# Kernel optimization log

Hardware: AMD Instinct MI355X
Metric: run time of the kernel (lower is better)

The kernel has to match this reference:

```python
import jax, jax.numpy as jnp
import numpy as np

H = 8          # n_heads
C_FACTOR = 3   # autocorrelation factor c
KS = 25        # series-decomp moving-average kernel


def series_decomp(x, ks=KS):
    # AvgPool1d(kernel=ks, stride=1, pad=ks//2), count_include_pad=True (torch default)
    p = ks // 2
    xp = jnp.pad(x, ((0, 0), (p, p), (0, 0)))            # [B, L+2p, D]
    cs = jnp.pad(jnp.cumsum(xp, axis=1), ((0, 0), (1, 0), (0, 0)))
    trend = (cs[:, ks:, :] - cs[:, :-ks, :]) / ks         # [B, L, D]
    return x - trend, trend


def auto_correlation(x, Wq, bq, Wk, bk, Wv, bv):
    B, L, D = x.shape
    d = D // H

    def proj(W, b):  # [B,L,D] -> [B,H,L,d]
        return (x @ W + b).reshape(B, L, H, d).transpose(0, 2, 1, 3)

    Q, K, V = proj(Wq, bq), proj(Wk, bk), proj(Wv, bv)
    Qf = jnp.fft.rfft(Q, axis=2)
    Kf = jnp.fft.rfft(K, axis=2)
    Corr = jnp.fft.irfft(Qf * jnp.conj(Kf), n=L, axis=2)  # [B,H,L,d]

    k = int(C_FACTOR * np.log(L))                         # topk = int(c*log(L))
    C2 = Corr.transpose(0, 1, 3, 2)                       # [B,H,d,L] - topk along lag axis per channel
    W_topk, I_topk = jax.lax.top_k(C2, k)                 # [B,H,d,k]
    W_topk = jax.nn.softmax(W_topk, axis=-1)

    # saturating shift: pos = min(delay + t, L-1)  (faithful to clamp(max=L-1))
    t = jnp.arange(L)
    pos = jnp.minimum(I_topk[..., None] + t[None, None, None, None, :], L - 1)  # [B,H,d,k,L]
    Vt = V.transpose(0, 1, 3, 2)                          # [B,H,d,L]
    gathered = jnp.take_along_axis(Vt[:, :, :, None, :], pos, axis=4)           # [B,H,d,k,L]
    R = jnp.einsum('bhdk,bhdkl->bhdl', W_topk, gathered)  # weighted aggregate over lags
    return R.transpose(0, 3, 1, 2).reshape(B, L, D)       # [B,L,D]


def setup_inputs() -> dict:
    key = jax.random.key(0)
    ks = jax.random.split(key, 11)
    B, L, D = 8, 1024, 512
    s = 0.02
    return {
        'x':  jax.random.normal(ks[0], (B, L, D), jnp.float32),
        'Wq': jax.random.normal(ks[1], (D, D), jnp.float32) * s,
        'bq': jnp.zeros((D,), jnp.float32),
        'Wk': jax.random.normal(ks[2], (D, D), jnp.float32) * s,
        'bk': jnp.zeros((D,), jnp.float32),
        'Wv': jax.random.normal(ks[3], (D, D), jnp.float32) * s,
        'bv': jnp.zeros((D,), jnp.float32),
        'W1': jax.random.normal(ks[4], (D, D), jnp.float32) * s,
        'b1': jnp.zeros((D,), jnp.float32),
        'W2': jax.random.normal(ks[5], (D, D), jnp.float32) * s,
        'b2': jnp.zeros((D,), jnp.float32),
    }


def reference(x, Wq, bq, Wk, bk, Wv, bv, W1, b1, W2, b2):
    attn = auto_correlation(x, Wq, bq, Wk, bk, Wv, bv)
    x_s, _ = series_decomp(attn + x)
    y = jax.nn.relu(x_s @ W1 + b1) @ W2 + b2              # FFN (dropout is identity in eval)
    x_s, _ = series_decomp(y + x_s)
    return x_s
```

## Files before the change

kernel.cpp:

```cpp
#include <hip/hip_runtime.h>
#include <math.h>

#define LL 1024
#define DD 512
#define NB 8
#define KTOP 20
#define SZ (8 * 512 * 1024)

typedef __attribute__((ext_vector_type(8))) short bf16x8;
typedef __attribute__((ext_vector_type(4))) float f32x4;
typedef __attribute__((ext_vector_type(4))) int i32x4;

__device__ __forceinline__ unsigned short f2bf(float f) {
  union { float f; unsigned u; } v; v.f = f;
  unsigned r = v.u + 0x7FFFu + ((v.u >> 16) & 1u);
  return (unsigned short)(r >> 16);
}
__device__ __forceinline__ float bf2f(unsigned short u) {
  union { unsigned u; float f; } v; v.u = ((unsigned)u) << 16;
  return v.f;
}

__device__ __forceinline__ void gload16(const void* g, void* l) {
  __builtin_amdgcn_global_load_lds(
      (const __attribute__((address_space(1))) unsigned int*)g,
      (__attribute__((address_space(3))) unsigned int*)l, 16, 0, 0);
}

__global__ __launch_bounds__(256) void k_prep(const float* __restrict__ x,
                                              float* __restrict__ xT,
                                              unsigned short* __restrict__ xb,
                                              const float* __restrict__ Wq,
                                              const float* __restrict__ Wk,
                                              const float* __restrict__ Wv,
                                              const float* __restrict__ W1,
                                              const float* __restrict__ W2,
                                              const float* __restrict__ bq,
                                              const float* __restrict__ bk,
                                              const float* __restrict__ bv,
                                              unsigned short* __restrict__ WqkvT,
                                              unsigned short* __restrict__ W1T,
                                              unsigned short* __restrict__ W2T,
                                              float* __restrict__ bqkv) {
  __shared__ float T[64][65];
  int bid = blockIdx.x;
  int tid = threadIdx.x;
  int lane = tid & 63, r4 = tid >> 6;
  if (bid < 1024) {
    int b = bid >> 7, c0 = ((bid >> 4) & 7) * 64, t0 = (bid & 15) * 64;
#pragma unroll
    for (int it = 0; it < 16; ++it) {
      int tl = it * 4 + r4;
      T[lane][tl] = x[((size_t)b * LL + t0 + tl) * DD + c0 + lane];
    }
    __syncthreads();
#pragma unroll
    for (int it = 0; it < 16; ++it) {
      int cl = it * 4 + r4;
      xT[((size_t)b * DD + c0 + cl) * LL + t0 + lane] = T[cl][lane];
    }
    int tl2 = tid >> 2, cq = (tid & 3) * 16;
    unsigned short* dxb = xb + ((size_t)b * LL + t0 + tl2) * DD + c0 + cq;
#pragma unroll
    for (int j = 0; j < 16; j += 4) {
      ushort4 u;
      u.x = f2bf(T[cq + j][tl2]);
      u.y = f2bf(T[cq + j + 1][tl2]);
      u.z = f2bf(T[cq + j + 2][tl2]);
      u.w = f2bf(T[cq + j + 3][tl2]);
      *(ushort4*)&dxb[j] = u;
    }
  } else {
    int pid = bid - 1024;
    int z = pid >> 6, n0 = ((pid >> 3) & 7) * 64, k0 = (pid & 7) * 64;
    const float* W = (z == 0) ? Wq : (z == 1) ? Wk : (z == 2) ? Wv : (z == 3) ? W1 : W2;
    unsigned short* dst = (z == 0) ? WqkvT
                        : (z == 1) ? (WqkvT + 512 * 512)
                        : (z == 2) ? (WqkvT + 1024 * 512)
                        : (z == 3) ? W1T : W2T;
#pragma unroll
    for (int it = 0; it < 16; ++it) {
      int kl = it * 4 + r4;
      T[lane][kl] = W[(size_t)(k0 + kl) * DD + n0 + lane];
    }
    __syncthreads();
    int n = tid >> 2, kq = (tid & 3) * 16;
    unsigned short* d = dst + (size_t)(n0 + n) * DD + k0 + kq;
#pragma unroll
    for (int j = 0; j < 16; j += 4) {
      ushort4 u;
      u.x = f2bf(T[n][kq + j]);
      u.y = f2bf(T[n][kq + j + 1]);
      u.z = f2bf(T[n][kq + j + 2]);
      u.w = f2bf(T[n][kq + j + 3]);
      *(ushort4*)&d[j] = u;
    }
    if (z == 4 && n0 == 0 && k0 == 0) {
      for (int i = tid; i < 1536; i += 256) {
        const float* s = (i < 512) ? bq : (i < 1024) ? bk : bv;
        bqkv[i] = s[i & 511];
      }
    }
  }
}

template <int MODE>
__global__ __launch_bounds__(256) void k_mfma(const unsigned short* __restrict__ Aptr,
                                              const unsigned short* __restrict__ Bt,
                                              const float* __restrict__ bias,
                                              const unsigned short* __restrict__ resbT,
                                              unsigned short* __restrict__ outU,
                                              float* __restrict__ outF, int gx) {
  __shared__ char smem[34816];
  unsigned short* As = (unsigned short*)smem;
  unsigned short* Bs = (unsigned short*)(smem + 16384);
  float* Cs = (float*)smem;

  int tid = threadIdx.x;
  int lane = tid & 63, wid = tid >> 6;
  int wr = wid & 1, wc = wid >> 1;

  int nwg = gridDim.x;
  int wg = blockIdx.x;
  int swz = (wg & 7) * (nwg >> 3) + (wg >> 3);
  int bix = swz % gx, biy = swz / gx;
  int n0 = bix * 128, m0 = biy * 128;
  int b = m0 >> 10, t0 = m0 & (LL - 1);

  f32x4 acc[4][4];
#pragma unroll
  for (int i = 0; i < 4; ++i)
#pragma unroll
    for (int j = 0; j < 4; ++j) acc[i][j] = (f32x4){0.f, 0.f, 0.f, 0.f};

  int srow = tid >> 3, sq = tid & 7;

  for (int k0 = 0; k0 < 512; k0 += 64) {
#pragma unroll
    for (int p = 0; p < 4; ++p) {
      int r = srow + p * 32;
      int dq = sq ^ (r & 7);
      gload16(Aptr + (size_t)(m0 + r) * 512 + k0 + dq * 8, &As[r * 64 + sq * 8]);
      gload16(Bt + (size_t)(n0 + r) * 512 + k0 + dq * 8, &Bs[r * 64 + sq * 8]);
    }
    __syncthreads();
#pragma unroll
    for (int ks = 0; ks < 2; ++ks) {
      bf16x8 af[4], bf[4];
      int fr = lane & 15, kq = lane >> 4;
#pragma unroll
      for (int mi = 0; mi < 4; ++mi) {
        int r = wr * 64 + mi * 16 + fr;
        af[mi] = *(bf16x8*)&As[r * 64 + ((ks * 4 + kq) ^ (r & 7)) * 8];
      }
#pragma unroll
      for (int ni = 0; ni < 4; ++ni) {
        int r = wc * 64 + ni * 16 + fr;
        bf[ni] = *(bf16x8*)&Bs[r * 64 + ((ks * 4 + kq) ^ (r & 7)) * 8];
      }
#pragma unroll
      for (int mi = 0; mi < 4; ++mi)
#pragma unroll
        for (int ni = 0; ni < 4; ++ni)
          acc[mi][ni] = __builtin_amdgcn_mfma_f32_16x16x32_bf16(af[mi], bf[ni], acc[mi][ni], 0, 0, 0);
    }
    __syncthreads();
  }

  if (MODE == 0 || MODE == 2) {
    const int LDc = 132;
    for (int p = 0; p < 2; ++p) {
      __syncthreads();
      if (MODE == 2) {
        int n = tid >> 2, mq = tid & 3;
        const unsigned short* rrow =
            resbT + ((size_t)(b * 512) + n0 + p * 64 + n) * LL + t0;
#pragma unroll
        for (int i = 0; i < 8; ++i) {
          int m = mq * 4 + i * 16;
          ushort4 u = *(const ushort4*)&rrow[m];
          float4 v;
          v.x = bf2f(u.x); v.y = bf2f(u.y); v.z = bf2f(u.z); v.w = bf2f(u.w);
          *(float4*)&Cs[n * LDc + m] = v;
        }
        __syncthreads();
      }
      if (wc == p) {
#pragma unroll
        for (int mi = 0; mi < 4; ++mi)
#pragma unroll
          for (int ni = 0; ni < 4; ++ni) {
            int nl = ni * 16 + (lane & 15);
            int ml = wr * 64 + mi * 16 + (lane >> 4) * 4;
            if (MODE == 2) {
              f32x4 cur = *(f32x4*)&Cs[nl * LDc + ml];
              cur += acc[mi][ni];
              *(f32x4*)&Cs[nl * LDc + ml] = cur;
            } else {
              *(f32x4*)&Cs[nl * LDc + ml] = acc[mi][ni];
            }
          }
      }
      __syncthreads();
      {
        int n = tid >> 2, mq = tid & 3;
        int ng = n0 + p * 64 + n;
        float bv = bias[ng];
        if (MODE == 0) {
          int sel = ng >> 9;
          unsigned short* drow =
              outU + ((size_t)sel * NB * 512 + b * 512 + (ng & 511)) * LL + t0;
#pragma unroll
          for (int i = 0; i < 8; ++i) {
            int m = mq * 4 + i * 16;
            float4 v = *(float4*)&Cs[n * LDc + m];
            ushort4 u;
            u.x = f2bf(v.x + bv); u.y = f2bf(v.y + bv);
            u.z = f2bf(v.z + bv); u.w = f2bf(v.w + bv);
            *(ushort4*)&drow[m] = u;
          }
        } else {
          float* drow = outF + ((size_t)b * 512 + ng) * LL + t0;
#pragma unroll
          for (int i = 0; i < 8; ++i) {
            int m = mq * 4 + i * 16;
            float4 v = *(float4*)&Cs[n * LDc + m];
            v.x += bv; v.y += bv; v.z += bv; v.w += bv;
            *(float4*)&drow[m] = v;
          }
        }
      }
    }
  } else {
    const int LDh = 68;
    for (int p = 0; p < 2; ++p) {
      __syncthreads();
      if (wc == p) {
#pragma unroll
        for (int mi = 0; mi < 4; ++mi)
#pragma unroll
          for (int ni = 0; ni < 4; ++ni) {
            int nl = ni * 16 + (lane & 15);
            int ml = wr * 64 + mi * 16 + (lane >> 4) * 4;
#pragma unroll
            for (int r = 0; r < 4; ++r) Cs[(ml + r) * LDh + nl] = acc[mi][ni][r];
          }
      }
      __syncthreads();
      {
        int m = tid >> 1, nh = tid & 1;
        unsigned short* drow =
            outU + (size_t)(m0 + m) * 512 + n0 + p * 64 + nh * 32;
#pragma unroll
        for (int c = 0; c < 8; ++c) {
          float4 v = *(float4*)&Cs[m * LDh + nh * 32 + c * 4];
          float4 bb = *(const float4*)&bias[n0 + p * 64 + nh * 32 + c * 4];
          v.x = fmaxf(v.x + bb.x, 0.f);
          v.y = fmaxf(v.y + bb.y, 0.f);
          v.z = fmaxf(v.z + bb.z, 0.f);
          v.w = fmaxf(v.w + bb.w, 0.f);
          ushort4 u;
          u.x = f2bf(v.x); u.y = f2bf(v.y); u.z = f2bf(v.z); u.w = f2bf(v.w);
          *(ushort4*)&drow[c * 4] = u;
        }
      }
    }
  }
}

__global__ __launch_bounds__(256) void k_autocorr(const unsigned short* __restrict__ Qbf,
                                                  const unsigned short* __restrict__ Kbf,
                                                  const unsigned short* __restrict__ Vbf,
                                                  const float* __restrict__ xT,
                                                  unsigned short* __restrict__ xsbT) {
  __shared__ char sm[20768];
  unsigned* QsW  = (unsigned*)sm;
  unsigned* KshW = (unsigned*)(sm + 4096);
  float* Vs2 = (float*)(sm + 12416);
  float* Cp  = (float*)(sm + 4608);
  float* wvs = (float*)(sm + 20608);
  int*   wis = (int*)(sm + 20688);
  float* Csp = (float*)sm;

  int tid = threadIdx.x;
  int lane = tid & 63, wave = tid >> 6;
  size_t base = (size_t)blockIdx.x * LL;

  {
    ushort4 q = *(const ushort4*)(Qbf + base + tid * 4);
    unsigned q0 = (unsigned)q.x | ((unsigned)q.y << 16);
    unsigned q1 = (unsigned)q.z | ((unsigned)q.w << 16);
    int Wa = 2 * tid;
    int Pa = Wa ^ (((Wa >> 5) & 3) << 2);
    uint2 qv; qv.x = q0; qv.y = q1;
    *(uint2*)&QsW[Pa] = qv;
    int Wb = 512 + 2 * tid;
    int Pb = Wb ^ (((Wb >> 5) & 3) << 2);
    *(uint2*)&QsW[Pb] = qv;

    ushort4 vv = *(const ushort4*)(Vbf + base + tid * 4);
    float4 vf;
    vf.x = bf2f(vv.x); vf.y = bf2f(vv.y); vf.z = bf2f(vv.z); vf.w = bf2f(vv.w);
    *(float4*)&Vs2[tid * 4] = vf;
    float vlast = bf2f(Vbf[base + 1023]);
    *(float4*)&Vs2[1024 + tid * 4] = make_float4(vlast, vlast, vlast, vlast);

    ushort4 kv = *(const ushort4*)(Kbf + base + tid * 4);
    unsigned w0 = (unsigned)kv.x | ((unsigned)kv.y << 16);
    unsigned w1 = (unsigned)kv.z | ((unsigned)kv.w << 16);
    unsigned wq = __shfl_up(w0, 1);
    unsigned wp = __shfl_up(w1, 1);
    if (lane == 0) {
      wq = *(const unsigned*)(Kbf + base + ((tid * 4 - 4) & (LL - 1)));
      wp = *(const unsigned*)(Kbf + base + ((tid * 4 - 2) & (LL - 1)));
    }
    int d = 8 + 2 * tid;
    uint2 u0; u0.x = w0;                      u0.y = w1;
    uint2 u1; u1.x = (wp >> 16) | (w0 << 16); u1.y = (w0 >> 16) | (w1 << 16);
    uint2 u2; u2.x = wp;                      u2.y = w0;
    uint2 u3; u3.x = (wq >> 16) | (wp << 16); u3.y = (wp >> 16) | (w0 << 16);
    *(uint2*)&KshW[d]        = u0;
    *(uint2*)&KshW[520 + d]  = u1;
    *(uint2*)&KshW[1040 + d] = u2;
    *(uint2*)&KshW[1560 + d] = u3;
    if (tid >= 224) {
      int q2 = tid - 224;
      int s = q2 >> 3, dd = q2 & 7;
      int p = 2 * dd - 16;
      unsigned short a = Kbf[base + ((p - s) & (LL - 1))];
      unsigned short b2 = Kbf[base + ((p + 1 - s) & (LL - 1))];
      KshW[s * 520 + dd] = (unsigned)a | ((unsigned)b2 << 16);
    }
  }
  __syncthreads();

  f32x4 acc = (f32x4){0.f, 0.f, 0.f, 0.f};
  int fr = lane & 15, kq = lane >> 4;
  int g = wave;
  int srow = fr & 3, fp = fr >> 2;
  int aW0 = 128 * g + 8 * fr + 4 * kq;
  int bD0 = srow * 520 + 8 + 4 * kq - 2 * fp;
#pragma unroll
  for (int ks = 0; ks < 32; ++ks) {
    int W = aW0 + 16 * ks;
    int Pw = W ^ (((W >> 5) & 3) << 2);
    bf16x8 av = *(const bf16x8*)&QsW[Pw];
    int bD = bD0 + 16 * ks;
    uint2 b01 = *(const uint2*)&KshW[bD];
    uint2 b23 = *(const uint2*)&KshW[bD + 2];
    union { unsigned u[4]; bf16x8 h; } ub;
    ub.u[0] = b01.x; ub.u[1] = b01.y; ub.u[2] = b23.x; ub.u[3] = b23.y;
    acc = __builtin_amdgcn_mfma_f32_16x16x32_bf16(av, ub.h, acc, 0, 0, 0);
  }
  __syncthreads();
#pragma unroll
  for (int r = 0; r < 4; ++r) {
    int tau = 256 * g + 64 * kq + 16 * r + fr;
    Cp[tau ^ (((tau >> 6) & 3) << 4)] = acc[r];
  }
  __syncthreads();

  int sel = blockIdx.x & 3;
  if (wave == sel) {
    float c0[16];
#pragma unroll
    for (int j = 0; j < 16; ++j) {
      int tau = 64 * j + lane;
      c0[j] = Cp[tau ^ (((tau >> 6) & 3) << 4)];
    }
    float lbest = c0[0];
    int lidx = 0;
#pragma unroll
    for (int m = 1; m < 16; ++m)
      if (c0[m] > lbest) { lbest = c0[m]; lidx = m; }

    float wv[KTOP];
    int wiR[KTOP];
#pragma unroll
    for (int s = 0; s < KTOP; ++s) {
      float best = lbest;
      int bidx = 64 * lidx + lane;
#pragma unroll
      for (int off = 32; off; off >>= 1) {
        float v2 = __shfl_xor(best, off);
        int i2 = __shfl_xor(bidx, off);
        if (v2 > best || (v2 == best && i2 < bidx)) { best = v2; bidx = i2; }
      }
      wv[s] = best;
      wiR[s] = bidx;
      int kill = ((bidx & 63) == lane) ? (bidx >> 6) : -1;
#pragma unroll
      for (int m = 0; m < 16; ++m)
        if (m == kill) c0[m] = -3.0e38f;
      lbest = c0[0];
      lidx = 0;
#pragma unroll
      for (int m = 1; m < 16; ++m)
        if (c0[m] > lbest) { lbest = c0[m]; lidx = m; }
    }
    float mx = wv[0];
#pragma unroll
    for (int m = 1; m < KTOP; ++m) mx = fmaxf(mx, wv[m]);
    float ssum = 0.f;
#pragma unroll
    for (int m = 0; m < KTOP; ++m) {
      wv[m] = __expf(wv[m] - mx);
      ssum += wv[m];
    }
    float inv = 1.f / ssum;
    if (lane == 0) {
#pragma unroll
      for (int m = 0; m < KTOP; ++m) {
        wvs[m] = wv[m] * inv;
        wis[m] = wiR[m];
      }
    }
  } else {
    int ft = (wave < sel ? wave : wave - 1) * 64 + lane;
    if (ft < 16) Csp[ft] = 0.f;
    else if (ft < 32) Csp[1040 + ft - 16] = 0.f;
  }
  __syncthreads();

  {
    float r[4];
#pragma unroll
    for (int i = 0; i < 4; ++i) r[i] = xT[base + tid + 256 * i];
#pragma unroll
    for (int k = 0; k < KTOP; ++k) {
      float w = wvs[k];
      int wi = wis[k];
#pragma unroll
      for (int i = 0; i < 4; ++i) r[i] += w * Vs2[wi + tid + 256 * i];
    }
#pragma unroll
    for (int i = 0; i < 4; ++i) Csp[16 + tid + 256 * i] = r[i];
  }
  __syncthreads();

  {
    int t0 = tid * 4;
    float buf[28];
#pragma unroll
    for (int qd = 0; qd < 7; ++qd)
      *(float4*)&buf[qd * 4] = *(const float4*)&Csp[t0 + 4 + qd * 4];
    float s = 0.f;
#pragma unroll
    for (int m = 0; m < 25; ++m) s += buf[m];
    ushort4 o;
    o.x = f2bf(buf[12] - s * (1.0f / 25.0f));
    s += buf[25] - buf[0];
    o.y = f2bf(buf[13] - s * (1.0f / 25.0f));
    s += buf[26] - buf[1];
    o.z = f2bf(buf[14] - s * (1.0f / 25.0f));
    s += buf[27] - buf[2];
    o.w = f2bf(buf[15] - s * (1.0f / 25.0f));
    *(ushort4*)&xsbT[base + t0] = o;
  }
}

__global__ __launch_bounds__(256) void k_castT(const unsigned short* __restrict__ src,
                                               unsigned short* __restrict__ dst) {
  __shared__ unsigned short T[64][68];
  int b = blockIdx.z;
  int t0 = blockIdx.x * 64, c0 = blockIdx.y * 64;
  int tid = threadIdx.x;
  int lane = tid & 63, r4 = tid >> 6;
#pragma unroll
  for (int it = 0; it < 16; ++it) {
    int cl = it * 4 + r4;
    T[lane][cl] = src[((size_t)b * 512 + c0 + cl) * LL + t0 + lane];
  }
  __syncthreads();
  int tl = tid >> 2, cq = (tid & 3) * 16;
  unsigned short* d = dst + ((size_t)b * LL + t0 + tl) * 512 + c0 + cq;
#pragma unroll
  for (int j = 0; j < 16; j += 4) {
    ushort4 u;
    u.x = T[tl][cq + j]; u.y = T[tl][cq + j + 1];
    u.z = T[tl][cq + j + 2]; u.w = T[tl][cq + j + 3];
    *(ushort4*)&d[j] = u;
  }
}

#define DCH 32
__global__ __launch_bounds__(256) void k_decomp2T(const float* __restrict__ s2T,
                                                  float* __restrict__ out) {
  __shared__ float T[DCH][289];
  int b = blockIdx.z, c0 = blockIdx.y * DCH, t0 = blockIdx.x * 256;
  int tid = threadIdx.x;
  {
    int row = tid >> 3, j0 = tid & 7;
    const float* src = s2T + ((size_t)b * 512 + c0 + row) * LL;
#pragma unroll
    for (int i = 0; i < 9; ++i) {
      int col = (j0 + i * 8) * 4;
      int t = t0 - 16 + col;
      float4 v = make_float4(0.f, 0.f, 0.f, 0.f);
      if (t >= 0 && t < LL) v = *(const float4*)&src[t];
      *(float4*)&T[row][col] = v;
    }
  }
  __syncthreads();
  int c = tid & 31, tg = tid >> 5;
  float sum = 0.f;
  int basec = tg * 32 + 4;
#pragma unroll
  for (int j = 0; j < 25; ++j) sum += T[c][basec + j];
  float* orow = out + ((size_t)b * LL + t0 + tg * 32) * 512 + c0 + c;
#pragma unroll 1
  for (int s = 0; s < 32; ++s) {
    float center = T[c][tg * 32 + 16 + s];
    orow[(size_t)s * 512] = center - sum * (1.f / 25.f);
    sum += T[c][basec + 25 + s] - T[c][basec + s];
  }
}

extern "C" void kernel_launch(void* const* d_in, const int* in_sizes, int n_in,
                              void* d_out, int out_size, void* d_ws, size_t ws_size,
                              hipStream_t stream) {
  const float* x  = (const float*)d_in[0];
  const float* Wq = (const float*)d_in[1];
  const float* bq = (const float*)d_in[2];
  const float* Wk = (const float*)d_in[3];
  const float* bk = (const float*)d_in[4];
  const float* Wv = (const float*)d_in[5];
  const float* bv = (const float*)d_in[6];
  const float* W1 = (const float*)d_in[7];
  const float* b1 = (const float*)d_in[8];
  const float* W2 = (const float*)d_in[9];
  const float* b2 = (const float*)d_in[10];
  float* out = (float*)d_out;
  char* w = (char*)d_ws;

  float* xT             = (float*)w;
  unsigned short* Qbf   = (unsigned short*)(w + (size_t)SZ * 4);
  unsigned short* Kbf   = Qbf + SZ;
  unsigned short* Vbf   = Kbf + SZ;
  unsigned short* WqkvT = (unsigned short*)(w + (size_t)SZ * 12);
  unsigned short* W1T   = WqkvT + 1536 * 512;
  unsigned short* W2T   = W1T + 512 * 512;
  float* bqkv           = (float*)(W2T + 512 * 512);
  unsigned short* xb    = (unsigned short*)(w + (size_t)SZ * 14);
  unsigned short* h1    = (unsigned short*)w;
  unsigned short* xsb   = (unsigned short*)(w + (size_t)SZ * 2);
  unsigned short* xsbT  = Qbf;
  float* s2T            = (float*)(w + (size_t)SZ * 6);

  k_prep<<<dim3(1344), 256, 0, stream>>>(x, xT, xb, Wq, Wk, Wv, W1, W2,
                                         bq, bk, bv, WqkvT, W1T, W2T, bqkv);

  k_mfma<0><<<dim3(768), 256, 0, stream>>>(xb, WqkvT, bqkv, nullptr, Qbf, nullptr, 12);

  k_autocorr<<<dim3(NB * DD), 256, 0, stream>>>(Qbf, Kbf, Vbf, xT, xsbT);

  k_castT<<<dim3(16, 8, NB), 256, 0, stream>>>(xsbT, xsb);

  k_mfma<1><<<dim3(256), 256, 0, stream>>>(xsb, W1T, b1, nullptr, h1, nullptr, 4);
  k_mfma<2><<<dim3(256), 256, 0, stream>>>(h1, W2T, b2, xsbT, nullptr, s2T, 4);

  k_decomp2T<<<dim3(4, 16, NB), 256, 0, stream>>>(s2T, out);
}
```

Measured before the change: 152.4 us.

## Shrink autocorr LDS/registers: read Q from global, bf16 residual, lane-parallel softmax

The autocorrelation kernel stops staging Q in shared memory and reads MFMA A-fragments straight from global (L1/L2), which cuts LDS to about 16.7KB. Top-k results go to LDS per step instead of register arrays, and the softmax is computed across lanes with shuffles. The kernel now asks for 8 blocks per CU to raise occupancy. The transposed residual x is stored as bf16 instead of fp32, which halves its write and read traffic but adds rounding error to the residual path.

After: 139.7 us. -8.3%, faster.

```diff
diff --git a/kernel.cpp b/kernel.cpp
--- a/kernel.cpp
+++ b/kernel.cpp
@@ -28,7 +28,7 @@
 }
 
 __global__ __launch_bounds__(256) void k_prep(const float* __restrict__ x,
-                                              float* __restrict__ xT,
+                                              unsigned short* __restrict__ xbT,
                                               unsigned short* __restrict__ xb,
                                               const float* __restrict__ Wq,
                                               const float* __restrict__ Wk,
@@ -57,7 +57,7 @@
 #pragma unroll
     for (int it = 0; it < 16; ++it) {
       int cl = it * 4 + r4;
-      xT[((size_t)b * DD + c0 + cl) * LL + t0 + lane] = T[cl][lane];
+      xbT[((size_t)b * DD + c0 + cl) * LL + t0 + lane] = f2bf(T[cl][lane]);
     }
     int tl2 = tid >> 2, cq = (tid & 3) * 16;
     unsigned short* dxb = xb + ((size_t)b * LL + t0 + tl2) * DD + c0 + cq;
@@ -268,36 +268,24 @@
   }
 }
 
-__global__ __launch_bounds__(256) void k_autocorr(const unsigned short* __restrict__ Qbf,
-                                                  const unsigned short* __restrict__ Kbf,
-                                                  const unsigned short* __restrict__ Vbf,
-                                                  const float* __restrict__ xT,
-                                                  unsigned short* __restrict__ xsbT) {
-  __shared__ char sm[20768];
-  unsigned* QsW  = (unsigned*)sm;
-  unsigned* KshW = (unsigned*)(sm + 4096);
-  float* Vs2 = (float*)(sm + 12416);
-  float* Cp  = (float*)(sm + 4608);
-  float* wvs = (float*)(sm + 20608);
-  int*   wis = (int*)(sm + 20688);
+__global__ __launch_bounds__(256, 8) void k_autocorr(const unsigned short* __restrict__ Qbf,
+                                                     const unsigned short* __restrict__ Kbf,
+                                                     const unsigned short* __restrict__ Vbf,
+                                                     const unsigned short* __restrict__ xbT,
+                                                     unsigned short* __restrict__ xsbT) {
+  __shared__ char sm[16672];
+  unsigned* KshW = (unsigned*)sm;
+  float* Vs2 = (float*)(sm + 8320);
+  float* wvs = (float*)(sm + 16512);
+  int*   wis = (int*)(sm + 16592);
   float* Csp = (float*)sm;
+  float* Cp  = (float*)(sm + 4224);
 
   int tid = threadIdx.x;
   int lane = tid & 63, wave = tid >> 6;
   size_t base = (size_t)blockIdx.x * LL;
 
   {
-    ushort4 q = *(const ushort4*)(Qbf + base + tid * 4);
-    unsigned q0 = (unsigned)q.x | ((unsigned)q.y << 16);
-    unsigned q1 = (unsigned)q.z | ((unsigned)q.w << 16);
-    int Wa = 2 * tid;
-    int Pa = Wa ^ (((Wa >> 5) & 3) << 2);
-    uint2 qv; qv.x = q0; qv.y = q1;
-    *(uint2*)&QsW[Pa] = qv;
-    int Wb = 512 + 2 * tid;
-    int Pb = Wb ^ (((Wb >> 5) & 3) << 2);
-    *(uint2*)&QsW[Pb] = qv;
-
     ushort4 vv = *(const ushort4*)(Vbf + base + tid * 4);
     float4 vf;
     vf.x = bf2f(vv.x); vf.y = bf2f(vv.y); vf.z = bf2f(vv.z); vf.w = bf2f(vv.w);
@@ -338,19 +326,19 @@
   int fr = lane & 15, kq = lane >> 4;
   int g = wave;
   int srow = fr & 3, fp = fr >> 2;
-  int aW0 = 128 * g + 8 * fr + 4 * kq;
+  int aE = (256 * g + 16 * fr + 8 * kq) & (LL - 1);
   int bD0 = srow * 520 + 8 + 4 * kq - 2 * fp;
+  const unsigned short* qp = Qbf + base;
 #pragma unroll
   for (int ks = 0; ks < 32; ++ks) {
-    int W = aW0 + 16 * ks;
-    int Pw = W ^ (((W >> 5) & 3) << 2);
-    bf16x8 av = *(const bf16x8*)&QsW[Pw];
+    bf16x8 av = *(const bf16x8*)(qp + aE);
     int bD = bD0 + 16 * ks;
     uint2 b01 = *(const uint2*)&KshW[bD];
     uint2 b23 = *(const uint2*)&KshW[bD + 2];
     union { unsigned u[4]; bf16x8 h; } ub;
     ub.u[0] = b01.x; ub.u[1] = b01.y; ub.u[2] = b23.x; ub.u[3] = b23.y;
     acc = __builtin_amdgcn_mfma_f32_16x16x32_bf16(av, ub.h, acc, 0, 0, 0);
+    aE = (aE + 32) & (LL - 1);
   }
   __syncthreads();
 #pragma unroll
@@ -374,9 +362,7 @@
     for (int m = 1; m < 16; ++m)
       if (c0[m] > lbest) { lbest = c0[m]; lidx = m; }
 
-    float wv[KTOP];
-    int wiR[KTOP];
-#pragma unroll
+#pragma unroll 1
     for (int s = 0; s < KTOP; ++s) {
       float best = lbest;
       int bidx = 64 * lidx + lane;
@@ -386,8 +372,7 @@
         int i2 = __shfl_xor(bidx, off);
         if (v2 > best || (v2 == best && i2 < bidx)) { best = v2; bidx = i2; }
       }
-      wv[s] = best;
-      wiR[s] = bidx;
+      if (lane == 0) { wvs[s] = best; wis[s] = bidx; }
       int kill = ((bidx & 63) == lane) ? (bidx >> 6) : -1;
 #pragma unroll
       for (int m = 0; m < 16; ++m)
@@ -398,23 +383,12 @@
       for (int m = 1; m < 16; ++m)
         if (c0[m] > lbest) { lbest = c0[m]; lidx = m; }
     }
-    float mx = wv[0];
-#pragma unroll
-    for (int m = 1; m < KTOP; ++m) mx = fmaxf(mx, wv[m]);
-    float ssum = 0.f;
-#pragma unroll
-    for (int m = 0; m < KTOP; ++m) {
-      wv[m] = __expf(wv[m] - mx);
-      ssum += wv[m];
-    }
-    float inv = 1.f / ssum;
-    if (lane == 0) {
-#pragma unroll
-      for (int m = 0; m < KTOP; ++m) {
-        wvs[m] = wv[m] * inv;
-        wis[m] = wiR[m];
-      }
-    }
+    float mx = wvs[0];
+    float e = (lane < KTOP) ? __expf(wvs[lane] - mx) : 0.f;
+    float ssum = e;
+#pragma unroll
+    for (int off = 32; off; off >>= 1) ssum += __shfl_xor(ssum, off);
+    if (lane < KTOP) wvs[lane] = e / ssum;
   } else {
     int ft = (wave < sel ? wave : wave - 1) * 64 + lane;
     if (ft < 16) Csp[ft] = 0.f;
@@ -425,7 +399,7 @@
   {
     float r[4];
 #pragma unroll
-    for (int i = 0; i < 4; ++i) r[i] = xT[base + tid + 256 * i];
+    for (int i = 0; i < 4; ++i) r[i] = bf2f(xbT[base + tid + 256 * i]);
 #pragma unroll
     for (int k = 0; k < KTOP; ++k) {
       float w = wvs[k];
@@ -533,7 +507,7 @@
   float* out = (float*)d_out;
   char* w = (char*)d_ws;
 
-  float* xT             = (float*)w;
+  unsigned short* xbT   = (unsigned short*)w;
   unsigned short* Qbf   = (unsigned short*)(w + (size_t)SZ * 4);
   unsigned short* Kbf   = Qbf + SZ;
   unsigned short* Vbf   = Kbf + SZ;
@@ -547,12 +521,12 @@
   unsigned short* xsbT  = Qbf;
   float* s2T            = (float*)(w + (size_t)SZ * 6);
 
-  k_prep<<<dim3(1344), 256, 0, stream>>>(x, xT, xb, Wq, Wk, Wv, W1, W2,
+  k_prep<<<dim3(1344), 256, 0, stream>>>(x, xbT, xb, Wq, Wk, Wv, W1, W2,
                                          bq, bk, bv, WqkvT, W1T, W2T, bqkv);
 
   k_mfma<0><<<dim3(768), 256, 0, stream>>>(xb, WqkvT, bqkv, nullptr, Qbf, nullptr, 12);
 
-  k_autocorr<<<dim3(NB * DD), 256, 0, stream>>>(Qbf, Kbf, Vbf, xT, xsbT);
+  k_autocorr<<<dim3(NB * DD), 256, 0, stream>>>(Qbf, Kbf, Vbf, xbT, xsbT);
 
   k_castT<<<dim3(16, 8, NB), 256, 0, stream>>>(xsbT, xsb);
 
```
